# Kernel optimization log

Measured on AMD Instinct MI355X. Metric: run time of the kernel, lower is better.

## Reference

```python
import jax, jax.numpy as jnp
import numpy as np

B, N, D, H, O, K, N_USER, C = 1, 4096, 64, 4, 64, 2, 4000, 2


def setup_inputs() -> dict:
    key = jax.random.key(0)
    ks = jax.random.split(key, 7)
    h = jax.random.normal(ks[0], (B, N, D), jnp.float32)
    # dense 0/1 adjacency per heterogeneous kind, with self-loops so no row is empty
    adj = jax.random.randint(ks[1], (K, B, N, N), 0, 2).astype(jnp.float32)
    hadj = jnp.maximum(adj, jnp.eye(N, dtype=jnp.float32))
    s = 1.0 / np.sqrt(D).astype(np.float32)
    w = jax.random.normal(ks[2], (K, H, D, O), jnp.float32) * s
    a_src = jax.random.normal(ks[3], (K, H, O, 1), jnp.float32) * (1.0 / np.sqrt(O).astype(np.float32))
    a_dst = jax.random.normal(ks[4], (K, H, O, 1), jnp.float32) * (1.0 / np.sqrt(O).astype(np.float32))
    fc_w = jax.random.normal(ks[5], (C, O * K), jnp.float32) * (1.0 / np.sqrt(O * K).astype(np.float32))
    fc_b = jnp.zeros((C,), jnp.float32)
    return {"h": h, "hadj": hadj, "w": w, "a_src": a_src, "a_dst": a_dst, "fc_w": fc_w, "fc_b": fc_b}


def _gat(h, adj, w_k, a_src_k, a_dst_k):
    # h: (B,N,D); adj: (B,N,N); w_k: (H,D,O); a_*: (H,O,1)
    h_prime = jnp.einsum('bnf,hfo->bhno', h, w_k)          # (B,H,N,O)
    t = jnp.tanh(h_prime)
    attn_src = jnp.einsum('bhno,hoi->bhni', t, a_src_k)    # (B,H,N,1)
    attn_dst = jnp.einsum('bhno,hoi->bhni', t, a_dst_k)    # (B,H,N,1)
    attn = attn_src + jnp.swapaxes(attn_dst, -1, -2)       # (B,H,N,N) broadcast add
    attn = jnp.where(attn >= 0, attn, 0.2 * attn)          # LeakyReLU(0.2)
    attn = jnp.where(adj[:, None] > 0, attn, -jnp.inf)     # dense mask
    attn = jax.nn.softmax(attn, axis=-1)                   # dropout is a no-op in eval
    out = jnp.einsum('bhnm,bhmo->bhno', attn, h_prime)     # (B,H,N,O)
    return out.mean(axis=1)                                # mean over heads -> (B,N,O)


def reference(h, hadj, w, a_src, a_dst, fc_w, fc_b):
    embs = []
    for k in range(K):  # small fixed loop over heterogeneous node kinds
        x = _gat(h, hadj[k], w[k], a_src[k], a_dst[k])
        embs.append(x[:, :N_USER])
    type_aware = jnp.concatenate(embs, axis=-1)            # (B, N_USER, K*O)
    logits = type_aware @ fc_w.T + fc_b                    # (B, N_USER, C)
    return jax.nn.log_softmax(logits, axis=-1)
```

## Files before the change

### kernel.cpp

```cpp
#include <hip/hip_runtime.h>
#include <math.h>

constexpr int KK = 2;
constexpr int HH = 4;
constexpr int NN = 4096;
constexpr int DD = 64;
constexpr int OO = 64;
constexpr int NU = 4000;
constexpr int CC = 2;
constexpr int JSPLIT = 4;
constexpr float LOG2E = 1.44269504088896340736f;

typedef float vf4 __attribute__((ext_vector_type(4)));
typedef float vf2 __attribute__((ext_vector_type(2)));

__device__ __forceinline__ float fexp2(float x) {
#if __has_builtin(__builtin_amdgcn_exp2f)
  return __builtin_amdgcn_exp2f(x);
#else
  return exp2f(x);
#endif
}
__device__ __forceinline__ float frcp(float x) {
#if __has_builtin(__builtin_amdgcn_rcpf)
  return __builtin_amdgcn_rcpf(x);
#else
  return 1.0f / x;
#endif
}
__device__ __forceinline__ float ftanh(float x) {
  float e = fexp2(x * (2.0f * LOG2E));
  return 1.0f - 2.0f * frcp(e + 1.0f);
}

__global__ __launch_bounds__(256) void gat_phase1(
    const float* __restrict__ hsrc, const float* __restrict__ w,
    const float* __restrict__ a_src, const float* __restrict__ a_dst,
    const float* __restrict__ fc_w,
    float* __restrict__ srcAA, float* __restrict__ Bp,
    float* __restrict__ B5p, float* __restrict__ g0p,
    float* __restrict__ g1p) {
  const int kh = blockIdx.y;
  const int k = kh >> 2;
  const int i0 = blockIdx.x * 64;
  const int tid = threadIdx.x;

  __shared__ float h_s[DD][68];
  __shared__ float w_s[DD][OO];
  __shared__ float part[4][64][17];

  {
    const vf4* wp = (const vf4*)(w + (size_t)kh * DD * OO);
    vf4* ws4 = (vf4*)w_s;
    for (int t = tid; t < DD * OO / 4; t += 256) ws4[t] = wp[t];
  }
  for (int t = tid; t < 1024; t += 256) {
    const int row = t >> 4;
    const int f4 = (t & 15) * 4;
    vf4 v = *(const vf4*)(hsrc + (size_t)(i0 + row) * DD + f4);
    h_s[f4 + 0][row] = v.x;
    h_s[f4 + 1][row] = v.y;
    h_s[f4 + 2][row] = v.z;
    h_s[f4 + 3][row] = v.w;
  }
  __syncthreads();

  const int og = tid & 15;
  const int rg = tid >> 4;
  const int o0 = og * 4;
  const int r0 = rg * 4;

  float hp[4][4];
#pragma unroll
  for (int j = 0; j < 4; ++j)
#pragma unroll
    for (int u = 0; u < 4; ++u) hp[j][u] = 0.0f;

#pragma unroll 8
  for (int f = 0; f < DD; ++f) {
    vf4 hv = *(const vf4*)&h_s[f][r0];
    vf4 wv = *(const vf4*)&w_s[f][o0];
    hp[0][0] = fmaf(hv.x, wv.x, hp[0][0]);
    hp[0][1] = fmaf(hv.x, wv.y, hp[0][1]);
    hp[0][2] = fmaf(hv.x, wv.z, hp[0][2]);
    hp[0][3] = fmaf(hv.x, wv.w, hp[0][3]);
    hp[1][0] = fmaf(hv.y, wv.x, hp[1][0]);
    hp[1][1] = fmaf(hv.y, wv.y, hp[1][1]);
    hp[1][2] = fmaf(hv.y, wv.z, hp[1][2]);
    hp[1][3] = fmaf(hv.y, wv.w, hp[1][3]);
    hp[2][0] = fmaf(hv.z, wv.x, hp[2][0]);
    hp[2][1] = fmaf(hv.z, wv.y, hp[2][1]);
    hp[2][2] = fmaf(hv.z, wv.z, hp[2][2]);
    hp[2][3] = fmaf(hv.z, wv.w, hp[2][3]);
    hp[3][0] = fmaf(hv.w, wv.x, hp[3][0]);
    hp[3][1] = fmaf(hv.w, wv.y, hp[3][1]);
    hp[3][2] = fmaf(hv.w, wv.z, hp[3][2]);
    hp[3][3] = fmaf(hv.w, wv.w, hp[3][3]);
  }

  float as[4], ad[4], f0[4], f1[4];
#pragma unroll
  for (int u = 0; u < 4; ++u) {
    as[u] = a_src[kh * OO + o0 + u];
    ad[u] = a_dst[kh * OO + o0 + u];
    f0[u] = fc_w[0 * (KK * OO) + k * OO + o0 + u];
    f1[u] = fc_w[1 * (KK * OO) + k * OO + o0 + u];
  }

#pragma unroll
  for (int j = 0; j < 4; ++j) {
    float sp = 0.0f, dp = 0.0f, g0 = 0.0f, g1 = 0.0f;
#pragma unroll
    for (int u = 0; u < 4; ++u) {
      float v = hp[j][u];
      float t = ftanh(v);
      sp = fmaf(t, as[u], sp);
      dp = fmaf(t, ad[u], dp);
      g0 = fmaf(v, f0[u], g0);
      g1 = fmaf(v, f1[u], g1);
    }
    part[0][r0 + j][og] = sp;
    part[1][r0 + j][og] = dp;
    part[2][r0 + j][og] = g0;
    part[3][r0 + j][og] = g1;
  }
  __syncthreads();

  {
    const int val = tid & 3;
    const int j2 = tid >> 2;
    const float* pr = &part[val][j2][0];
    vf4 s0 = *(const vf4*)(pr + 0);
    vf4 s1 = *(const vf4*)(pr + 4);
    vf4 s2 = *(const vf4*)(pr + 8);
    vf4 s3 = *(const vf4*)(pr + 12);
    vf4 t4 = s0 + s1 + s2 + s3;
    float sum = t4.x + t4.y + t4.z + t4.w;
    const size_t idx = (size_t)kh * NN + i0 + j2;
    if (val == 0) {
      float sp = sum * LOG2E;
      vf2 v = {fexp2(sp), fexp2(0.2f * sp)};
      *(vf2*)(srcAA + idx * 2) = v;
    } else if (val == 1) {
      float dp = sum * LOG2E;
      Bp[idx] = fexp2(dp);
      B5p[idx] = fexp2(0.2f * dp);
    } else if (val == 2) {
      g0p[idx] = sum;
    } else {
      g1p[idx] = sum;
    }
  }
}

__global__ __launch_bounds__(64) void gat_phase2(
    const float* __restrict__ adj, const float* __restrict__ srcAA,
    const float* __restrict__ Bp, const float* __restrict__ B5p,
    const float* __restrict__ g0p, const float* __restrict__ g1p,
    float* __restrict__ P) {
  const int k = blockIdx.y >> 2;
  const int chunk = blockIdx.y & 3;
  const int r0 = blockIdx.x * 4;
  const int lane = threadIdx.x;

  float A[4][4], A5[4][4];
#pragma unroll
  for (int h = 0; h < 4; ++h) {
    const float* base = srcAA + ((size_t)(k * HH + h) * NN + r0) * 2;
#pragma unroll
    for (int r = 0; r < 4; ++r) {
      A[r][h] = base[r * 2 + 0];
      A5[r][h] = base[r * 2 + 1];
    }
  }

  float l[4][4], a0[4][4], a1[4][4];
#pragma unroll
  for (int r = 0; r < 4; ++r)
#pragma unroll
    for (int h = 0; h < 4; ++h) {
      l[r][h] = 0.0f;
      a0[r][h] = 0.0f;
      a1[r][h] = 0.0f;
    }

  const float* adjk = adj + (size_t)k * NN * NN;
  const int jw = chunk * 1024 + lane * 4;

  vf4 avc[4], avn[4];
#pragma unroll
  for (int r = 0; r < 4; ++r)
    avc[r] = *(const vf4*)(adjk + (size_t)(r0 + r) * NN + jw);

#pragma unroll 1
  for (int t = 0; t < 4; ++t) {
    const int j = jw + t * 256;
    if (t < 3) {
#pragma unroll
      for (int r = 0; r < 4; ++r)
        avn[r] = *(const vf4*)(adjk + (size_t)(r0 + r) * NN + j + 256);
    }
    size_t pb = (size_t)(k * HH + 0) * NN + j;
    vf4 bC = *(const vf4*)(Bp + pb);
    vf4 b5C = *(const vf4*)(B5p + pb);
    vf4 g0C = *(const vf4*)(g0p + pb);
    vf4 g1C = *(const vf4*)(g1p + pb);
#pragma unroll
    for (int h = 0; h < 4; ++h) {
      vf4 b = bC, b5 = b5C, g0 = g0C, g1 = g1C;
      if (h < 3) {
        size_t pn = (size_t)(k * HH + h + 1) * NN + j;
        bC = *(const vf4*)(Bp + pn);
        b5C = *(const vf4*)(B5p + pn);
        g0C = *(const vf4*)(g0p + pn);
        g1C = *(const vf4*)(g1p + pn);
      }
      vf2 blo = {b.x, b.y}, bhi = {b.z, b.w};
      vf2 b5lo = {b5.x, b5.y}, b5hi = {b5.z, b5.w};
#pragma unroll
      for (int r = 0; r < 4; ++r) {
        vf2 elo = __builtin_elementwise_max(blo * A[r][h], b5lo * A5[r][h]);
        vf2 ehi = __builtin_elementwise_max(bhi * A[r][h], b5hi * A5[r][h]);
        float p0 = elo.x * avc[r].x;
        float p1 = elo.y * avc[r].y;
        float p2 = ehi.x * avc[r].z;
        float p3 = ehi.y * avc[r].w;
        l[r][h] += (p0 + p1) + (p2 + p3);
        a0[r][h] = fmaf(p0, g0.x, fmaf(p1, g0.y, fmaf(p2, g0.z, fmaf(p3, g0.w, a0[r][h]))));
        a1[r][h] = fmaf(p0, g1.x, fmaf(p1, g1.y, fmaf(p2, g1.z, fmaf(p3, g1.w, a1[r][h]))));
      }
    }
#pragma unroll
    for (int r = 0; r < 4; ++r) avc[r] = avn[r];
  }

#pragma unroll
  for (int r = 0; r < 4; ++r)
#pragma unroll
    for (int h = 0; h < 4; ++h) {
      float x0 = l[r][h], x1 = a0[r][h], x2 = a1[r][h];
#pragma unroll
      for (int off = 32; off > 0; off >>= 1) {
        x0 += __shfl_xor(x0, off, 64);
        x1 += __shfl_xor(x1, off, 64);
        x2 += __shfl_xor(x2, off, 64);
      }
      l[r][h] = x0;
      a0[r][h] = x1;
      a1[r][h] = x2;
    }

  if (lane == 0) {
#pragma unroll
    for (int r = 0; r < 4; ++r)
#pragma unroll
      for (int h = 0; h < 4; ++h) {
        size_t base =
            (((size_t)(k * JSPLIT + chunk) * HH + h) * 3) * NU + (r0 + r);
        P[base] = l[r][h];
        P[base + NU] = a0[r][h];
        P[base + 2 * (size_t)NU] = a1[r][h];
      }
  }
}

__global__ __launch_bounds__(256) void gat_phase3(
    const float* __restrict__ P, const float* __restrict__ fc_b,
    float* __restrict__ out) {
  const int i = blockIdx.x * 256 + threadIdx.x;
  if (i >= NU) return;
  float l0 = fc_b[0], l1 = fc_b[1];
#pragma unroll
  for (int k = 0; k < KK; ++k) {
#pragma unroll
    for (int q = 0; q < HH; ++q) {
      float ls = 0.0f, a0 = 0.0f, a1 = 0.0f;
#pragma unroll
      for (int ch = 0; ch < JSPLIT; ++ch) {
        size_t b = (((size_t)(k * JSPLIT + ch) * HH + q) * 3) * NU + i;
        ls += P[b];
        a0 += P[b + NU];
        a1 += P[b + 2 * (size_t)NU];
      }
      float inv = 1.0f / ls;
      l0 = fmaf(0.25f * a0, inv, l0);
      l1 = fmaf(0.25f * a1, inv, l1);
    }
  }
  float m = fmaxf(l0, l1);
  float lse = m + logf(expf(l0 - m) + expf(l1 - m));
  out[i * CC + 0] = l0 - lse;
  out[i * CC + 1] = l1 - lse;
}

extern "C" void kernel_launch(void* const* d_in, const int* in_sizes, int n_in,
                              void* d_out, int out_size, void* d_ws, size_t ws_size,
                              hipStream_t stream) {
  const float* hsrc  = (const float*)d_in[0];
  const float* hadj  = (const float*)d_in[1];
  const float* w     = (const float*)d_in[2];
  const float* a_src = (const float*)d_in[3];
  const float* a_dst = (const float*)d_in[4];
  const float* fc_w  = (const float*)d_in[5];
  const float* fc_b  = (const float*)d_in[6];
  float* out = (float*)d_out;

  char* ws = (char*)d_ws;
  float* srcAA = (float*)(ws + 0);
  float* Bp    = (float*)(ws + 262144);
  float* B5p   = (float*)(ws + 393216);
  float* g0p   = (float*)(ws + 524288);
  float* g1p   = (float*)(ws + 655360);
  float* P     = (float*)(ws + 786432);

  dim3 g1(NN / 64, KK * HH);
  gat_phase1<<<g1, 256, 0, stream>>>(hsrc, w, a_src, a_dst, fc_w,
                                     srcAA, Bp, B5p, g0p, g1p);
  dim3 g2(NU / 4, KK * JSPLIT);
  gat_phase2<<<g2, 64, 0, stream>>>(hadj, srcAA, Bp, B5p, g0p, g1p, P);
  gat_phase3<<<(NU + 255) / 256, 256, 0, stream>>>(P, fc_b, out);
}
```

Measured before the change: 235.7 us.

## Precompress adjacency into wave ballot bitmasks and consume them in attention pass

A new pre-pass reads the dense float adjacency once and packs it into 64-bit ballot masks, one per wave-lane group. The attention-accumulation kernel then reads these compact masks through scalar loads and selects values with v_cndmask instead of streaming float adjacency vectors and multiplying by them. Phase2 is also reorganized to loop over heads with 8 rows per block, instead of keeping all heads in registers for 4 rows. The pre-pass still reads the full adjacency, including rows beyond the user count, and adds a kernel launch. This trades raw traffic for lower register pressure and lighter inner-loop loads.

```diff
diff --git a/kernel.cpp b/kernel.cpp
--- a/kernel.cpp
+++ b/kernel.cpp
@@ -13,6 +13,7 @@
 
 typedef float vf4 __attribute__((ext_vector_type(4)));
 typedef float vf2 __attribute__((ext_vector_type(2)));
+typedef unsigned long long u64;
 
 __device__ __forceinline__ float fexp2(float x) {
 #if __has_builtin(__builtin_amdgcn_exp2f)
@@ -31,6 +32,33 @@
 __device__ __forceinline__ float ftanh(float x) {
   float e = fexp2(x * (2.0f * LOG2E));
   return 1.0f - 2.0f * frcp(e + 1.0f);
+}
+__device__ __forceinline__ float selbit(float e, u64 m) {
+  float r;
+  asm("v_cndmask_b32 %0, 0, %1, %2" : "=v"(r) : "v"(e), "s"(m));
+  return r;
+}
+
+__global__ __launch_bounds__(256) void gat_mask(
+    const float* __restrict__ adj, u64* __restrict__ maskbuf) {
+  const int wid = blockIdx.x * 4 + (threadIdx.x >> 6);
+  const int lane = threadIdx.x & 63;
+#pragma unroll
+  for (int it = 0; it < 4; ++it) {
+    const int task = wid * 4 + it;
+    vf4 v = *(const vf4*)(adj + (size_t)task * 256 + lane * 4);
+    u64 m0 = __ballot(v.x > 0.5f);
+    u64 m1 = __ballot(v.y > 0.5f);
+    u64 m2 = __ballot(v.z > 0.5f);
+    u64 m3 = __ballot(v.w > 0.5f);
+    if (lane == 0) {
+      u64* dst = maskbuf + (size_t)task * 4;
+      dst[0] = m0;
+      dst[1] = m1;
+      dst[2] = m2;
+      dst[3] = m3;
+    }
+  }
 }
 
 __global__ __launch_bounds__(256) void gat_phase1(
@@ -154,113 +182,89 @@
 }
 
 __global__ __launch_bounds__(64) void gat_phase2(
-    const float* __restrict__ adj, const float* __restrict__ srcAA,
+    const u64* __restrict__ maskbuf, const float* __restrict__ srcAA,
     const float* __restrict__ Bp, const float* __restrict__ B5p,
     const float* __restrict__ g0p, const float* __restrict__ g1p,
     float* __restrict__ P) {
   const int k = blockIdx.y >> 2;
   const int chunk = blockIdx.y & 3;
-  const int r0 = blockIdx.x * 4;
+  const int r0 = blockIdx.x * 8;
   const int lane = threadIdx.x;
 
-  float A[4][4], A5[4][4];
-#pragma unroll
-  for (int h = 0; h < 4; ++h) {
-    const float* base = srcAA + ((size_t)(k * HH + h) * NN + r0) * 2;
-#pragma unroll
-    for (int r = 0; r < 4; ++r) {
-      A[r][h] = base[r * 2 + 0];
-      A5[r][h] = base[r * 2 + 1];
-    }
-  }
-
-  float l[4][4], a0[4][4], a1[4][4];
-#pragma unroll
-  for (int r = 0; r < 4; ++r)
-#pragma unroll
-    for (int h = 0; h < 4; ++h) {
-      l[r][h] = 0.0f;
-      a0[r][h] = 0.0f;
-      a1[r][h] = 0.0f;
-    }
-
-  const float* adjk = adj + (size_t)k * NN * NN;
-  const int jw = chunk * 1024 + lane * 4;
-
-  vf4 avc[4], avn[4];
-#pragma unroll
-  for (int r = 0; r < 4; ++r)
-    avc[r] = *(const vf4*)(adjk + (size_t)(r0 + r) * NN + jw);
-
 #pragma unroll 1
-  for (int t = 0; t < 4; ++t) {
-    const int j = jw + t * 256;
-    if (t < 3) {
-#pragma unroll
-      for (int r = 0; r < 4; ++r)
-        avn[r] = *(const vf4*)(adjk + (size_t)(r0 + r) * NN + j + 256);
-    }
-    size_t pb = (size_t)(k * HH + 0) * NN + j;
-    vf4 bC = *(const vf4*)(Bp + pb);
-    vf4 b5C = *(const vf4*)(B5p + pb);
-    vf4 g0C = *(const vf4*)(g0p + pb);
-    vf4 g1C = *(const vf4*)(g1p + pb);
-#pragma unroll
-    for (int h = 0; h < 4; ++h) {
-      vf4 b = bC, b5 = b5C, g0 = g0C, g1 = g1C;
-      if (h < 3) {
-        size_t pn = (size_t)(k * HH + h + 1) * NN + j;
-        bC = *(const vf4*)(Bp + pn);
-        b5C = *(const vf4*)(B5p + pn);
-        g0C = *(const vf4*)(g0p + pn);
-        g1C = *(const vf4*)(g1p + pn);
-      }
+  for (int h = 0; h < HH; ++h) {
+    float A[8], A5[8];
+    {
+      const float* base = srcAA + ((size_t)(k * HH + h) * NN + r0) * 2;
+#pragma unroll
+      for (int r = 0; r < 8; ++r) {
+        A[r] = base[r * 2 + 0];
+        A5[r] = base[r * 2 + 1];
+      }
+    }
+
+    float l[8], a0[8], a1[8];
+#pragma unroll
+    for (int r = 0; r < 8; ++r) {
+      l[r] = 0.0f;
+      a0[r] = 0.0f;
+      a1[r] = 0.0f;
+    }
+
+#pragma unroll
+    for (int t = 0; t < 4; ++t) {
+      const int j = chunk * 1024 + t * 256;
+      const size_t pb = (size_t)(k * HH + h) * NN + j + lane * 4;
+      vf4 b = *(const vf4*)(Bp + pb);
+      vf4 b5 = *(const vf4*)(B5p + pb);
+      vf4 g0 = *(const vf4*)(g0p + pb);
+      vf4 g1 = *(const vf4*)(g1p + pb);
       vf2 blo = {b.x, b.y}, bhi = {b.z, b.w};
       vf2 b5lo = {b5.x, b5.y}, b5hi = {b5.z, b5.w};
-#pragma unroll
-      for (int r = 0; r < 4; ++r) {
-        vf2 elo = __builtin_elementwise_max(blo * A[r][h], b5lo * A5[r][h]);
-        vf2 ehi = __builtin_elementwise_max(bhi * A[r][h], b5hi * A5[r][h]);
-        float p0 = elo.x * avc[r].x;
-        float p1 = elo.y * avc[r].y;
-        float p2 = ehi.x * avc[r].z;
-        float p3 = ehi.y * avc[r].w;
-        l[r][h] += (p0 + p1) + (p2 + p3);
-        a0[r][h] = fmaf(p0, g0.x, fmaf(p1, g0.y, fmaf(p2, g0.z, fmaf(p3, g0.w, a0[r][h]))));
-        a1[r][h] = fmaf(p0, g1.x, fmaf(p1, g1.y, fmaf(p2, g1.z, fmaf(p3, g1.w, a1[r][h]))));
-      }
-    }
-#pragma unroll
-    for (int r = 0; r < 4; ++r) avc[r] = avn[r];
-  }
-
-#pragma unroll
-  for (int r = 0; r < 4; ++r)
-#pragma unroll
-    for (int h = 0; h < 4; ++h) {
-      float x0 = l[r][h], x1 = a0[r][h], x2 = a1[r][h];
+      const int tileIdx = chunk * 4 + t;
+#pragma unroll
+      for (int r = 0; r < 8; ++r) {
+        const u64* mp =
+            maskbuf + (((size_t)(k * NN + r0 + r) * 16) + tileIdx) * 4;
+        const u64 m0 = mp[0], m1 = mp[1], m2 = mp[2], m3 = mp[3];
+        vf2 elo = __builtin_elementwise_max(blo * A[r], b5lo * A5[r]);
+        vf2 ehi = __builtin_elementwise_max(bhi * A[r], b5hi * A5[r]);
+        float p0 = selbit(elo.x, m0);
+        float p1 = selbit(elo.y, m1);
+        float p2 = selbit(ehi.x, m2);
+        float p3 = selbit(ehi.y, m3);
+        l[r] += (p0 + p1) + (p2 + p3);
+        a0[r] = fmaf(p0, g0.x,
+                     fmaf(p1, g0.y, fmaf(p2, g0.z, fmaf(p3, g0.w, a0[r]))));
+        a1[r] = fmaf(p0, g1.x,
+                     fmaf(p1, g1.y, fmaf(p2, g1.z, fmaf(p3, g1.w, a1[r]))));
+      }
+    }
+
+#pragma unroll
+    for (int r = 0; r < 8; ++r) {
+      float x0 = l[r], x1 = a0[r], x2 = a1[r];
 #pragma unroll
       for (int off = 32; off > 0; off >>= 1) {
         x0 += __shfl_xor(x0, off, 64);
         x1 += __shfl_xor(x1, off, 64);
         x2 += __shfl_xor(x2, off, 64);
       }
-      l[r][h] = x0;
-      a0[r][h] = x1;
-      a1[r][h] = x2;
-    }
-
-  if (lane == 0) {
-#pragma unroll
-    for (int r = 0; r < 4; ++r)
-#pragma unroll
-      for (int h = 0; h < 4; ++h) {
-        size_t base =
-            (((size_t)(k * JSPLIT + chunk) * HH + h) * 3) * NU + (r0 + r);
-        P[base] = l[r][h];
-        P[base + NU] = a0[r][h];
-        P[base + 2 * (size_t)NU] = a1[r][h];
-      }
+      l[r] = x0;
+      a0[r] = x1;
+      a1[r] = x2;
+    }
+
+    if (lane == 0) {
+      size_t base =
+          (((size_t)(k * JSPLIT + chunk) * HH + h) * 3) * NU + r0;
+#pragma unroll
+      for (int r = 0; r < 8; ++r) {
+        P[base + r] = l[r];
+        P[base + NU + r] = a0[r];
+        P[base + 2 * (size_t)NU + r] = a1[r];
+      }
+    }
   }
 }
 
@@ -312,11 +316,13 @@
   float* g0p   = (float*)(ws + 524288);
   float* g1p   = (float*)(ws + 655360);
   float* P     = (float*)(ws + 786432);
-
+  u64*   maskbuf = (u64*)(ws + 2359296);
+
+  gat_mask<<<8192, 256, 0, stream>>>(hadj, maskbuf);
   dim3 g1(NN / 64, KK * HH);
   gat_phase1<<<g1, 256, 0, stream>>>(hsrc, w, a_src, a_dst, fc_w,
                                      srcAA, Bp, B5p, g0p, g1p);
-  dim3 g2(NU / 4, KK * JSPLIT);
-  gat_phase2<<<g2, 64, 0, stream>>>(hadj, srcAA, Bp, B5p, g0p, g1p, P);
+  dim3 g2(NU / 8, KK * JSPLIT);
+  gat_phase2<<<g2, 64, 0, stream>>>(maskbuf, srcAA, Bp, B5p, g0p, g1p, P);
   gat_phase3<<<(NU + 255) / 256, 256, 0, stream>>>(P, fc_b, out);
 }
```

New measurement: 259.7 us. 10.2% more time.

## Shrink per-block tiles in both GAT phases and halve the column split

Applied to the files above, without the earlier changes.

Phase 1 now handles 16 rows per block instead of 64, with one row per thread, which gives four times as many blocks. Phase 2 processes 2 destination rows per wavefront instead of 4 and splits the columns in 2 instead of 4, drops the software prefetch of adjacency and per-head vectors, and adds an occupancy hint to launch_bounds. The goal is more parallelism and lower register pressure on the bandwidth-bound adjacency stream. In exchange, each Bp/B5p/g0p/g1p load is reused across fewer rows, so that traffic roughly doubles, and the explicit load pipelining is gone.

```diff
diff --git a/kernel.cpp b/kernel.cpp
--- a/kernel.cpp
+++ b/kernel.cpp
@@ -8,7 +8,8 @@
 constexpr int OO = 64;
 constexpr int NU = 4000;
 constexpr int CC = 2;
-constexpr int JSPLIT = 4;
+constexpr int JSPLIT = 2;
+constexpr int JCHUNK = NN / JSPLIT;
 constexpr float LOG2E = 1.44269504088896340736f;
 
 typedef float vf4 __attribute__((ext_vector_type(4)));
@@ -42,21 +43,22 @@
     float* __restrict__ g1p) {
   const int kh = blockIdx.y;
   const int k = kh >> 2;
-  const int i0 = blockIdx.x * 64;
+  const int i0 = blockIdx.x * 16;
   const int tid = threadIdx.x;
 
-  __shared__ float h_s[DD][68];
   __shared__ float w_s[DD][OO];
-  __shared__ float part[4][64][17];
+  __shared__ float h_s[DD][20];
+  __shared__ float part[4][16][17];
 
   {
     const vf4* wp = (const vf4*)(w + (size_t)kh * DD * OO);
     vf4* ws4 = (vf4*)w_s;
+#pragma unroll
     for (int t = tid; t < DD * OO / 4; t += 256) ws4[t] = wp[t];
   }
-  for (int t = tid; t < 1024; t += 256) {
-    const int row = t >> 4;
-    const int f4 = (t & 15) * 4;
+  {
+    const int row = tid >> 4;
+    const int f4 = (tid & 15) * 4;
     vf4 v = *(const vf4*)(hsrc + (size_t)(i0 + row) * DD + f4);
     h_s[f4 + 0][row] = v.x;
     h_s[f4 + 1][row] = v.y;
@@ -66,77 +68,49 @@
   __syncthreads();
 
   const int og = tid & 15;
-  const int rg = tid >> 4;
+  const int r = tid >> 4;
   const int o0 = og * 4;
-  const int r0 = rg * 4;
-
-  float hp[4][4];
-#pragma unroll
-  for (int j = 0; j < 4; ++j)
-#pragma unroll
-    for (int u = 0; u < 4; ++u) hp[j][u] = 0.0f;
-
-#pragma unroll 8
+
+  vf4 hp = (vf4)(0.0f);
+#pragma unroll 16
   for (int f = 0; f < DD; ++f) {
-    vf4 hv = *(const vf4*)&h_s[f][r0];
+    float hv = h_s[f][r];
     vf4 wv = *(const vf4*)&w_s[f][o0];
-    hp[0][0] = fmaf(hv.x, wv.x, hp[0][0]);
-    hp[0][1] = fmaf(hv.x, wv.y, hp[0][1]);
-    hp[0][2] = fmaf(hv.x, wv.z, hp[0][2]);
-    hp[0][3] = fmaf(hv.x, wv.w, hp[0][3]);
-    hp[1][0] = fmaf(hv.y, wv.x, hp[1][0]);
-    hp[1][1] = fmaf(hv.y, wv.y, hp[1][1]);
-    hp[1][2] = fmaf(hv.y, wv.z, hp[1][2]);
-    hp[1][3] = fmaf(hv.y, wv.w, hp[1][3]);
-    hp[2][0] = fmaf(hv.z, wv.x, hp[2][0]);
-    hp[2][1] = fmaf(hv.z, wv.y, hp[2][1]);
-    hp[2][2] = fmaf(hv.z, wv.z, hp[2][2]);
-    hp[2][3] = fmaf(hv.z, wv.w, hp[2][3]);
-    hp[3][0] = fmaf(hv.w, wv.x, hp[3][0]);
-    hp[3][1] = fmaf(hv.w, wv.y, hp[3][1]);
-    hp[3][2] = fmaf(hv.w, wv.z, hp[3][2]);
-    hp[3][3] = fmaf(hv.w, wv.w, hp[3][3]);
-  }
-
-  float as[4], ad[4], f0[4], f1[4];
-#pragma unroll
-  for (int u = 0; u < 4; ++u) {
-    as[u] = a_src[kh * OO + o0 + u];
-    ad[u] = a_dst[kh * OO + o0 + u];
-    f0[u] = fc_w[0 * (KK * OO) + k * OO + o0 + u];
-    f1[u] = fc_w[1 * (KK * OO) + k * OO + o0 + u];
-  }
-
-#pragma unroll
-  for (int j = 0; j < 4; ++j) {
+    hp.x = fmaf(hv, wv.x, hp.x);
+    hp.y = fmaf(hv, wv.y, hp.y);
+    hp.z = fmaf(hv, wv.z, hp.z);
+    hp.w = fmaf(hv, wv.w, hp.w);
+  }
+
+  {
     float sp = 0.0f, dp = 0.0f, g0 = 0.0f, g1 = 0.0f;
 #pragma unroll
     for (int u = 0; u < 4; ++u) {
-      float v = hp[j][u];
+      float v = (u == 0) ? hp.x : (u == 1) ? hp.y : (u == 2) ? hp.z : hp.w;
       float t = ftanh(v);
-      sp = fmaf(t, as[u], sp);
-      dp = fmaf(t, ad[u], dp);
-      g0 = fmaf(v, f0[u], g0);
-      g1 = fmaf(v, f1[u], g1);
-    }
-    part[0][r0 + j][og] = sp;
-    part[1][r0 + j][og] = dp;
-    part[2][r0 + j][og] = g0;
-    part[3][r0 + j][og] = g1;
+      sp = fmaf(t, a_src[kh * OO + o0 + u], sp);
+      dp = fmaf(t, a_dst[kh * OO + o0 + u], dp);
+      g0 = fmaf(v, fc_w[0 * (KK * OO) + k * OO + o0 + u], g0);
+      g1 = fmaf(v, fc_w[1 * (KK * OO) + k * OO + o0 + u], g1);
+    }
+    part[0][r][og] = sp;
+    part[1][r][og] = dp;
+    part[2][r][og] = g0;
+    part[3][r][og] = g1;
   }
   __syncthreads();
 
-  {
+  if (tid < 64) {
     const int val = tid & 3;
-    const int j2 = tid >> 2;
-    const float* pr = &part[val][j2][0];
+    const int row = tid >> 2;
+    const float* pr = &part[val][row][0];
     vf4 s0 = *(const vf4*)(pr + 0);
     vf4 s1 = *(const vf4*)(pr + 4);
     vf4 s2 = *(const vf4*)(pr + 8);
     vf4 s3 = *(const vf4*)(pr + 12);
     vf4 t4 = s0 + s1 + s2 + s3;
     float sum = t4.x + t4.y + t4.z + t4.w;
-    const size_t idx = (size_t)kh * NN + i0 + j2;
+    const size_t idx = (size_t)kh * NN + i0 + row;
     if (val == 0) {
       float sp = sum * LOG2E;
       vf2 v = {fexp2(sp), fexp2(0.2f * sp)};
@@ -153,30 +127,30 @@
   }
 }
 
-__global__ __launch_bounds__(64) void gat_phase2(
+__global__ __launch_bounds__(64, 8) void gat_phase2(
     const float* __restrict__ adj, const float* __restrict__ srcAA,
     const float* __restrict__ Bp, const float* __restrict__ B5p,
     const float* __restrict__ g0p, const float* __restrict__ g1p,
     float* __restrict__ P) {
-  const int k = blockIdx.y >> 2;
-  const int chunk = blockIdx.y & 3;
-  const int r0 = blockIdx.x * 4;
+  const int k = blockIdx.y >> 1;
+  const int chunk = blockIdx.y & 1;
+  const int r0 = blockIdx.x * 2;
   const int lane = threadIdx.x;
 
-  float A[4][4], A5[4][4];
+  float A[2][4], A5[2][4];
 #pragma unroll
   for (int h = 0; h < 4; ++h) {
     const float* base = srcAA + ((size_t)(k * HH + h) * NN + r0) * 2;
 #pragma unroll
-    for (int r = 0; r < 4; ++r) {
+    for (int r = 0; r < 2; ++r) {
       A[r][h] = base[r * 2 + 0];
       A5[r][h] = base[r * 2 + 1];
     }
   }
 
-  float l[4][4], a0[4][4], a1[4][4];
-#pragma unroll
-  for (int r = 0; r < 4; ++r)
+  float l[2][4], a0[2][4], a1[2][4];
+#pragma unroll
+  for (int r = 0; r < 2; ++r)
 #pragma unroll
     for (int h = 0; h < 4; ++h) {
       l[r][h] = 0.0f;
@@ -184,58 +158,44 @@
       a1[r][h] = 0.0f;
     }
 
-  const float* adjk = adj + (size_t)k * NN * NN;
-  const int jw = chunk * 1024 + lane * 4;
-
-  vf4 avc[4], avn[4];
-#pragma unroll
-  for (int r = 0; r < 4; ++r)
-    avc[r] = *(const vf4*)(adjk + (size_t)(r0 + r) * NN + jw);
+  const float* adjr0 =
+      adj + (size_t)k * NN * NN + (size_t)r0 * NN + chunk * JCHUNK + lane * 4;
+  const float* adjr1 = adjr0 + NN;
+  const size_t pbase = chunk * JCHUNK + lane * 4;
 
 #pragma unroll 1
-  for (int t = 0; t < 4; ++t) {
-    const int j = jw + t * 256;
-    if (t < 3) {
-#pragma unroll
-      for (int r = 0; r < 4; ++r)
-        avn[r] = *(const vf4*)(adjk + (size_t)(r0 + r) * NN + j + 256);
-    }
-    size_t pb = (size_t)(k * HH + 0) * NN + j;
-    vf4 bC = *(const vf4*)(Bp + pb);
-    vf4 b5C = *(const vf4*)(B5p + pb);
-    vf4 g0C = *(const vf4*)(g0p + pb);
-    vf4 g1C = *(const vf4*)(g1p + pb);
+  for (int t = 0; t < 8; ++t) {
+    vf4 av0 = *(const vf4*)(adjr0 + t * 256);
+    vf4 av1 = *(const vf4*)(adjr1 + t * 256);
 #pragma unroll
     for (int h = 0; h < 4; ++h) {
-      vf4 b = bC, b5 = b5C, g0 = g0C, g1 = g1C;
-      if (h < 3) {
-        size_t pn = (size_t)(k * HH + h + 1) * NN + j;
-        bC = *(const vf4*)(Bp + pn);
-        b5C = *(const vf4*)(B5p + pn);
-        g0C = *(const vf4*)(g0p + pn);
-        g1C = *(const vf4*)(g1p + pn);
-      }
+      const size_t pb = (size_t)(k * HH + h) * NN + pbase + t * 256;
+      vf4 b = *(const vf4*)(Bp + pb);
+      vf4 b5 = *(const vf4*)(B5p + pb);
+      vf4 g0 = *(const vf4*)(g0p + pb);
+      vf4 g1 = *(const vf4*)(g1p + pb);
       vf2 blo = {b.x, b.y}, bhi = {b.z, b.w};
       vf2 b5lo = {b5.x, b5.y}, b5hi = {b5.z, b5.w};
 #pragma unroll
-      for (int r = 0; r < 4; ++r) {
+      for (int r = 0; r < 2; ++r) {
         vf2 elo = __builtin_elementwise_max(blo * A[r][h], b5lo * A5[r][h]);
         vf2 ehi = __builtin_elementwise_max(bhi * A[r][h], b5hi * A5[r][h]);
-        float p0 = elo.x * avc[r].x;
-        float p1 = elo.y * avc[r].y;
-        float p2 = ehi.x * avc[r].z;
-        float p3 = ehi.y * avc[r].w;
+        vf4 av = (r == 0) ? av0 : av1;
+        float p0 = elo.x * av.x;
+        float p1 = elo.y * av.y;
+        float p2 = ehi.x * av.z;
+        float p3 = ehi.y * av.w;
         l[r][h] += (p0 + p1) + (p2 + p3);
-        a0[r][h] = fmaf(p0, g0.x, fmaf(p1, g0.y, fmaf(p2, g0.z, fmaf(p3, g0.w, a0[r][h]))));
-        a1[r][h] = fmaf(p0, g1.x, fmaf(p1, g1.y, fmaf(p2, g1.z, fmaf(p3, g1.w, a1[r][h]))));
-      }
-    }
-#pragma unroll
-    for (int r = 0; r < 4; ++r) avc[r] = avn[r];
-  }
-
-#pragma unroll
-  for (int r = 0; r < 4; ++r)
+        a0[r][h] = fmaf(p0, g0.x,
+                        fmaf(p1, g0.y, fmaf(p2, g0.z, fmaf(p3, g0.w, a0[r][h]))));
+        a1[r][h] = fmaf(p0, g1.x,
+                        fmaf(p1, g1.y, fmaf(p2, g1.z, fmaf(p3, g1.w, a1[r][h]))));
+      }
+    }
+  }
+
+#pragma unroll
+  for (int r = 0; r < 2; ++r)
 #pragma unroll
     for (int h = 0; h < 4; ++h) {
       float x0 = l[r][h], x1 = a0[r][h], x2 = a1[r][h];
@@ -252,7 +212,7 @@
 
   if (lane == 0) {
 #pragma unroll
-    for (int r = 0; r < 4; ++r)
+    for (int r = 0; r < 2; ++r)
 #pragma unroll
       for (int h = 0; h < 4; ++h) {
         size_t base =
@@ -313,10 +273,10 @@
   float* g1p   = (float*)(ws + 655360);
   float* P     = (float*)(ws + 786432);
 
-  dim3 g1(NN / 64, KK * HH);
+  dim3 g1(NN / 16, KK * HH);
   gat_phase1<<<g1, 256, 0, stream>>>(hsrc, w, a_src, a_dst, fc_w,
                                      srcAA, Bp, B5p, g0p, g1p);
-  dim3 g2(NU / 4, KK * JSPLIT);
+  dim3 g2(NU / 2, KK * JSPLIT);
   gat_phase2<<<g2, 64, 0, stream>>>(hadj, srcAA, Bp, B5p, g0p, g1p, P);
   gat_phase3<<<(NU + 255) / 256, 256, 0, stream>>>(P, fc_b, out);
 }
```

Result: slower. 293.9 us (+24.7%).
